# Kernel optimization log

Measured on AMD Instinct MI355X. Metric: run time of the kernel, lower is better.

Reference implementation:

```python
import jax, jax.numpy as jnp
import numpy as np

N_ENT = 200000  # entities per graph (sr and tg)
E = 4_000_000   # triples per graph
R_SR, R_TG, D = 1000, 1200, 128


def _cosine_sim_nbyn(a, b):
    a = a * jax.lax.rsqrt(jnp.sum(a * a, -1, keepdims=True) + 1e-8)
    b = b * jax.lax.rsqrt(jnp.sum(b * b, -1, keepdims=True) + 1e-8)
    return a @ b.T


def _relation_weighting(a, b):
    # pad to square, cosine similarity, max-pool rows/cols (MuGNN RelationWeighting)
    ra, rb = a.shape[0], b.shape[0]
    n = max(ra, rb)
    a_p = jnp.pad(a, ((0, n - ra), (0, 0)))
    b_p = jnp.pad(b, ((0, n - rb), (0, 0)))
    sim = _cosine_sim_nbyn(a_p, b_p)  # [n, n]
    return jnp.max(sim, axis=1)[:ra], jnp.max(sim, axis=0)[:rb]


def _normalize_adj(rows, cols, vals, n):
    # symmetric normalization D^-1/2 A D^-1/2 on COO values
    deg = jax.ops.segment_sum(vals, rows, num_segments=n)
    d_is = jnp.where(deg > 0, jax.lax.rsqrt(jnp.maximum(deg, 1e-12)), 0.0)
    return vals * d_is[rows] * d_is[cols]


def _adjacency_side(head, tail, conf, imp, pca, n):
    # g_func_template: elementwise product of the three aligned sparse matrices
    vals = conf * imp * pca
    # + unit (identity) matrix, then normalize; coords = [edges ; diagonal]
    diag = jnp.arange(n)
    rows = jnp.concatenate([head, diag])
    cols = jnp.concatenate([tail, diag])
    allv = jnp.concatenate([vals, jnp.ones((n,), vals.dtype)])
    return _normalize_adj(rows, cols, allv, n)  # [E+n] COO values


def setup_inputs() -> dict:
    key = jax.random.key(0)
    ks = jax.random.split(key, 14)
    return {
        "rel_emb_sr": jax.random.normal(ks[0], (R_SR, D), jnp.float32),
        "rel_emb_tg": jax.random.normal(ks[1], (R_TG, D), jnp.float32),
        "conf_sr": jax.random.uniform(ks[2], (E,), jnp.float32),
        "imp_sr": jax.random.uniform(ks[3], (E,), jnp.float32),
        "pca_sr": jax.random.uniform(ks[4], (E,), jnp.float32),
        "conf_tg": jax.random.uniform(ks[5], (E,), jnp.float32),
        "imp_tg": jax.random.uniform(ks[6], (E,), jnp.float32),
        "pca_tg": jax.random.uniform(ks[7], (E,), jnp.float32),
        "head_sr": jax.random.randint(ks[8], (E,), 0, N_ENT),
        "tail_sr": jax.random.randint(ks[9], (E,), 0, N_ENT),
        "relation_sr": jax.random.randint(ks[10], (E,), 0, R_SR),
        "head_tg": jax.random.randint(ks[11], (E,), 0, N_ENT),
        "tail_tg": jax.random.randint(ks[12], (E,), 0, N_ENT),
        "relation_tg": jax.random.randint(ks[13], (E,), 0, R_TG),
    }


def reference(rel_emb_sr, rel_emb_tg, conf_sr, imp_sr, pca_sr,
              conf_tg, imp_tg, pca_tg,
              head_sr, tail_sr, relation_sr, head_tg, tail_tg, relation_tg):
    # relation weighting (computed in the original forward; g_func_template
    # discards the gathered relation attention, so relation_sr/tg do not
    # affect the adjacency values)
    rw_sr, rw_tg = _relation_weighting(rel_emb_sr, rel_emb_tg)
    adj_sr = _adjacency_side(head_sr, tail_sr, conf_sr, imp_sr, pca_sr, N_ENT)
    adj_tg = _adjacency_side(head_tg, tail_tg, conf_tg, imp_tg, pca_tg, N_ENT)
    # adjacency returned as normalized COO values on constant coords
    return adj_sr, adj_tg, rw_sr, rw_tg
```

## Files before the change

### kernel.cpp

```cpp
#include <hip/hip_runtime.h>
#include <stdint.h>

#define N_ENT 200000
#define NEDGE 4000000
#define RSR 1000
#define RTG 1200
#define DIM 128

#define NBUCK 400
#define BUCKSZ 500
#define CAP 11264
#define CHUNK 4096
#define NE4 (NEDGE / 4)
#define NBLK 977
#define PER (NEDGE + N_ENT)
#define PER4 (PER / 4)
#define ATILES 16
#define BTILES 19

__device__ __forceinline__ uint32_t to_bf16(float x) {
    uint32_t u = __float_as_uint(x);
    return (u + 0x7FFFu + ((u >> 16) & 1u)) >> 16;
}


__global__ void prep_kernel(const float* __restrict__ emb_sr, const float* __restrict__ emb_tg,
                            float* __restrict__ an, float* __restrict__ bn,
                            float* __restrict__ dis, unsigned* __restrict__ gcount) {
    int blk = blockIdx.x, t = threadIdx.x;
    if (blk < RSR + RTG) {
        const float* src; float* dst; int row;
        if (blk < RSR) { src = emb_sr; dst = an; row = blk; }
        else           { src = emb_tg; dst = bn; row = blk - RSR; }
        float x = src[row * DIM + t];
        __shared__ float sh[DIM];
        sh[t] = x * x;
        __syncthreads();
        for (int off = 64; off > 0; off >>= 1) {
            if (t < off) sh[t] += sh[t + off];
            __syncthreads();
        }
        dst[row * DIM + t] = x * rsqrtf(sh[0] + 1e-8f);
        if (blk == 0)
            for (int i = t; i < 2 * NBUCK; i += DIM) gcount[i] = 0;
    } else {
        int b = blk - (RSR + RTG);
        for (int i = t; i < 1000; i += DIM) dis[b * 1000 + i] = 1.0f;
    }
}


__global__ __launch_bounds__(256) void passA_kernel(
        const float* __restrict__ conf_sr, const float* __restrict__ imp_sr,
        const float* __restrict__ pca_sr,
        const float* __restrict__ conf_tg, const float* __restrict__ imp_tg,
        const float* __restrict__ pca_tg,
        const int* __restrict__ head_sr, const int* __restrict__ head_tg,
        float* __restrict__ out_sr, float* __restrict__ out_tg,
        unsigned* __restrict__ gcount, unsigned* __restrict__ regions) {
    __shared__ unsigned cnt[NBUCK];
    __shared__ unsigned scan_a[512];
    __shared__ unsigned scan_b[512];
    __shared__ unsigned offs[NBUCK];
    __shared__ unsigned gdst[NBUCK];
    __shared__ unsigned stage[CHUNK];
    __shared__ unsigned short aux[CHUNK];

    const int t = threadIdx.x;
    const int side = (int)blockIdx.x >= NBLK;
    const int blk = side ? blockIdx.x - NBLK : blockIdx.x;
    const float4* conf4 = (const float4*)(side ? conf_tg : conf_sr);
    const float4* imp4  = (const float4*)(side ? imp_tg  : imp_sr);
    const float4* pca4  = (const float4*)(side ? pca_tg  : pca_sr);
    const int4*   head4 = (const int4*)(side ? head_tg : head_sr);
    float4*       o4    = (float4*)(side ? out_tg : out_sr);

    for (int i = t; i < NBUCK; i += 256) cnt[i] = 0;
    __syncthreads();

    int bkt[16];
    unsigned rec[16], rnk[16];
#pragma unroll
    for (int i = 0; i < 4; i++) {
        int q = blk * 1024 + t + i * 256;
        if (q < NE4) {
            float4 cf = conf4[q], im = imp4[q], pc = pca4[q];
            int4 hh = head4[q];
            float4 v = make_float4(cf.x * im.x * pc.x, cf.y * im.y * pc.y,
                                   cf.z * im.z * pc.z, cf.w * im.w * pc.w);
            o4[q] = v;
            const int hs[4] = {hh.x, hh.y, hh.z, hh.w};
            const float vs[4] = {v.x, v.y, v.z, v.w};
#pragma unroll
            for (int j = 0; j < 4; j++) {
                int bb = hs[j] / BUCKSZ;
                bkt[i * 4 + j] = bb;
                rec[i * 4 + j] = ((unsigned)(hs[j] - bb * BUCKSZ) << 16) | to_bf16(vs[j]);
                rnk[i * 4 + j] = atomicAdd(&cnt[bb], 1u);
            }
        } else {
#pragma unroll
            for (int j = 0; j < 4; j++) bkt[i * 4 + j] = -1;
        }
    }
    __syncthreads();

    for (int i = t; i < 512; i += 256) scan_a[i] = (i < NBUCK) ? cnt[i] : 0;
    __syncthreads();
    unsigned* src = scan_a;
    unsigned* dst = scan_b;
    for (int s = 1; s < 512; s <<= 1) {
        for (int i = t; i < 512; i += 256)
            dst[i] = src[i] + (i >= s ? src[i - s] : 0u);
        __syncthreads();
        unsigned* tmp = src; src = dst; dst = tmp;
    }
    for (int i = t; i < NBUCK; i += 256) offs[i] = src[i] - cnt[i];
    __syncthreads();

#pragma unroll
    for (int i = 0; i < 16; i++) {
        if (bkt[i] >= 0) {
            unsigned pos = offs[bkt[i]] + rnk[i];
            stage[pos] = rec[i];
            aux[pos] = (unsigned short)bkt[i];
        }
    }
    for (int i = t; i < NBUCK; i += 256) {
        unsigned gb = atomicAdd(&gcount[side * NBUCK + i], cnt[i]);
        gdst[i] = (unsigned)(side * NBUCK + i) * CAP + gb - offs[i];
    }
    __syncthreads();

    unsigned total = src[NBUCK - 1];
    for (int i = t; i < (int)total; i += 256) {
        unsigned b = aux[i];
        unsigned d = gdst[b] + i;
        if (d < (unsigned)(side * NBUCK + b + 1) * CAP) regions[d] = stage[i];
    }
}


__global__ __launch_bounds__(256) void passB_kernel(const unsigned* __restrict__ regions,
                                                    const unsigned* __restrict__ gcount,
                                                    float* __restrict__ dis) {
    __shared__ float bins[BUCKSZ];
    int t = threadIdx.x;
    for (int i = t; i < BUCKSZ; i += 256) bins[i] = 1.0f;
    __syncthreads();
    unsigned n = gcount[blockIdx.x];
    if (n > CAP) n = CAP;
    const unsigned* rp = regions + (size_t)blockIdx.x * CAP;
    for (unsigned i = t; i < n; i += 256) {
        unsigned rec = rp[i];
        atomicAdd(&bins[rec >> 16], __uint_as_float((rec & 0xFFFFu) << 16));
    }
    __syncthreads();
    float* dout = dis + (size_t)blockIdx.x * BUCKSZ;
    for (int i = t; i < BUCKSZ; i += 256) dout[i] = rsqrtf(bins[i]);
}


__global__ void scatter_atomic_kernel(
        const float* __restrict__ conf_sr, const float* __restrict__ imp_sr,
        const float* __restrict__ pca_sr,
        const float* __restrict__ conf_tg, const float* __restrict__ imp_tg,
        const float* __restrict__ pca_tg,
        const int* __restrict__ head_sr, const int* __restrict__ head_tg,
        float* __restrict__ out_sr, float* __restrict__ out_tg,
        float* __restrict__ deg) {
    int e = blockIdx.x * blockDim.x + threadIdx.x;
    if (e < NEDGE) {
        float v = conf_sr[e] * imp_sr[e] * pca_sr[e];
        out_sr[e] = v;
        unsafeAtomicAdd(&deg[head_sr[e]], v);
    } else if (e < 2 * NEDGE) {
        int i = e - NEDGE;
        float v = conf_tg[i] * imp_tg[i] * pca_tg[i];
        out_tg[i] = v;
        unsafeAtomicAdd(&deg[N_ENT + head_tg[i]], v);
    }
}

__global__ void rsqrt_kernel(float* __restrict__ dis) {
    int i = blockIdx.x * blockDim.x + threadIdx.x;
    if (i < 2 * N_ENT) dis[i] = rsqrtf(dis[i]);
}


__global__ __launch_bounds__(256) void finalize_kernel(
        const int* __restrict__ head_sr, const int* __restrict__ tail_sr,
        const int* __restrict__ head_tg, const int* __restrict__ tail_tg,
        const float* __restrict__ dis, float* __restrict__ out) {
    int idx = blockIdx.x * blockDim.x + threadIdx.x;
    if (idx >= 2 * PER4) return;
    int side = idx >= PER4 ? 1 : 0;
    int q = side ? idx - PER4 : idx;
    const float* dg = dis + (size_t)side * N_ENT;
    float4* o = (float4*)(out + (size_t)side * PER);
    if (q < NE4) {
        const int4* hd = (const int4*)(side ? head_tg : head_sr);
        const int4* tl = (const int4*)(side ? tail_tg : tail_sr);
        int4 hh = hd[q];
        int4 tt = tl[q];
        float4 v = o[q];
        v.x *= dg[hh.x] * dg[tt.x];
        v.y *= dg[hh.y] * dg[tt.y];
        v.z *= dg[hh.z] * dg[tt.z];
        v.w *= dg[hh.w] * dg[tt.w];
        o[q] = v;
    } else {
        float4 d = ((const float4*)dg)[q - NE4];
        o[q] = make_float4(d.x * d.x, d.y * d.y, d.z * d.z, d.w * d.w);
    }
}


__global__ __launch_bounds__(256) void pools_tiles_kernel(
        const float* __restrict__ an, const float* __restrict__ bn,
        float* __restrict__ rowpart, float* __restrict__ colpart) {
    __shared__ float sA[64][132];
    __shared__ float sB[64][133];
    __shared__ float rr[64][17];
    __shared__ float cc[64][17];
    int t = threadIdx.x;
    int atile = blockIdx.x % ATILES;
    int btile = blockIdx.x / ATILES;
    for (int idx = t; idx < 64 * 32; idx += 256) {
        int row = idx >> 5, k4 = idx & 31;
        int ga = atile * 64 + row;
        float4 va = (ga < RSR) ? ((const float4*)(an + ga * DIM))[k4]
                               : make_float4(0.f, 0.f, 0.f, 0.f);
        *(float4*)&sA[row][k4 * 4] = va;
        int gb = btile * 64 + row;
        float4 vb = (gb < RTG) ? ((const float4*)(bn + gb * DIM))[k4]
                               : make_float4(0.f, 0.f, 0.f, 0.f);
        sB[row][k4 * 4 + 0] = vb.x; sB[row][k4 * 4 + 1] = vb.y;
        sB[row][k4 * 4 + 2] = vb.z; sB[row][k4 * 4 + 3] = vb.w;
    }
    __syncthreads();
    int tx = t & 15, ty = t >> 4;
    float acc[4][4] = {};
    for (int k4 = 0; k4 < 32; k4++) {
        float4 a4[4];
#pragma unroll
        for (int r = 0; r < 4; r++) a4[r] = *(const float4*)&sA[ty * 4 + r][k4 * 4];
#pragma unroll
        for (int kk = 0; kk < 4; kk++) {
            float bv[4];
#pragma unroll
            for (int c = 0; c < 4; c++) bv[c] = sB[tx * 4 + c][k4 * 4 + kk];
            float av[4];
#pragma unroll
            for (int r = 0; r < 4; r++)
                av[r] = kk == 0 ? a4[r].x : kk == 1 ? a4[r].y : kk == 2 ? a4[r].z : a4[r].w;
#pragma unroll
            for (int r = 0; r < 4; r++)
#pragma unroll
                for (int c = 0; c < 4; c++) acc[r][c] = fmaf(av[r], bv[c], acc[r][c]);
        }
    }
    float rm[4] = {-1e30f, -1e30f, -1e30f, -1e30f};
    float cm[4] = {-1e30f, -1e30f, -1e30f, -1e30f};
#pragma unroll
    for (int r = 0; r < 4; r++)
#pragma unroll
        for (int c = 0; c < 4; c++) {
            bool jok = (btile * 64 + tx * 4 + c) < RTG;
            rm[r] = fmaxf(rm[r], jok ? acc[r][c] : -1e30f);
            cm[c] = fmaxf(cm[c], acc[r][c]);
        }
#pragma unroll
    for (int r = 0; r < 4; r++) rr[ty * 4 + r][tx] = rm[r];
#pragma unroll
    for (int c = 0; c < 4; c++) cc[tx * 4 + c][ty] = cm[c];
    __syncthreads();
    if (t < 64) {
        float m = rr[t][0];
        for (int x = 1; x < 16; x++) m = fmaxf(m, rr[t][x]);
        rowpart[btile * 1024 + atile * 64 + t] = m;
        float m2 = cc[t][0];
        for (int x = 1; x < 16; x++) m2 = fmaxf(m2, cc[t][x]);
        colpart[atile * 1216 + btile * 64 + t] = m2;
    }
}


__global__ void rw_reduce_kernel(const float* __restrict__ rowpart,
                                 const float* __restrict__ colpart,
                                 float* __restrict__ rw_sr, float* __restrict__ rw_tg) {
    int idx = blockIdx.x * blockDim.x + threadIdx.x;
    if (idx < 1024) {
        if (idx < RSR) {
            float m = -1e30f;
            for (int b = 0; b < BTILES; b++) m = fmaxf(m, rowpart[b * 1024 + idx]);
            rw_sr[idx] = m;
        }
    } else {
        int j = idx - 1024;
        if (j < RTG) {
            float m = -1e30f;
            for (int a = 0; a < ATILES; a++) m = fmaxf(m, colpart[a * 1216 + j]);
            rw_tg[j] = fmaxf(m, 0.0f);
        }
    }
}


extern "C" void kernel_launch(void* const* d_in, const int* in_sizes, int n_in,
                              void* d_out, int out_size, void* d_ws, size_t ws_size,
                              hipStream_t stream) {
    const float* rel_emb_sr = (const float*)d_in[0];
    const float* rel_emb_tg = (const float*)d_in[1];
    const float* conf_sr = (const float*)d_in[2];
    const float* imp_sr  = (const float*)d_in[3];
    const float* pca_sr  = (const float*)d_in[4];
    const float* conf_tg = (const float*)d_in[5];
    const float* imp_tg  = (const float*)d_in[6];
    const float* pca_tg  = (const float*)d_in[7];
    const int* head_sr = (const int*)d_in[8];
    const int* tail_sr = (const int*)d_in[9];
    const int* head_tg = (const int*)d_in[11];
    const int* tail_tg = (const int*)d_in[12];

    float* out = (float*)d_out;
    float* out_sr = out;
    float* out_tg = out + PER;
    float* rw_sr  = out + 2 * (size_t)PER;
    float* rw_tg  = rw_sr + RSR;

    float* ws = (float*)d_ws;
    float* an  = ws;
    float* bn  = an + RSR * DIM;
    float* dis = bn + RTG * DIM;
    unsigned* gcount  = (unsigned*)(dis + 2 * N_ENT);
    unsigned* regions = gcount + 2 * NBUCK;
    float* rowpart = (float*)(regions + (size_t)2 * NBUCK * CAP);
    float* colpart = rowpart + BTILES * 1024;

    size_t need = ((size_t)(RSR * DIM + RTG * DIM + 2 * N_ENT + 2 * NBUCK) +
                   (size_t)2 * NBUCK * CAP + BTILES * 1024 + ATILES * 1216) * 4;
    bool bucketed = ws_size >= need;

    hipLaunchKernelGGL(prep_kernel, dim3(RSR + RTG + 400), dim3(DIM), 0, stream,
                       rel_emb_sr, rel_emb_tg, an, bn, dis, gcount);

    if (bucketed) {
        hipLaunchKernelGGL(passA_kernel, dim3(2 * NBLK), dim3(256), 0, stream,
                           conf_sr, imp_sr, pca_sr, conf_tg, imp_tg, pca_tg,
                           head_sr, head_tg, out_sr, out_tg, gcount, regions);
        hipLaunchKernelGGL(passB_kernel, dim3(2 * NBUCK), dim3(256), 0, stream,
                           regions, gcount, dis);
    } else {
        hipLaunchKernelGGL(scatter_atomic_kernel, dim3((2 * NEDGE + 255) / 256), dim3(256),
                           0, stream,
                           conf_sr, imp_sr, pca_sr, conf_tg, imp_tg, pca_tg,
                           head_sr, head_tg, out_sr, out_tg, dis);
        hipLaunchKernelGGL(rsqrt_kernel, dim3((2 * N_ENT + 255) / 256), dim3(256), 0, stream,
                           dis);
    }

    hipLaunchKernelGGL(pools_tiles_kernel, dim3(ATILES * BTILES), dim3(256), 0, stream,
                       an, bn, rowpart, colpart);
    hipLaunchKernelGGL(rw_reduce_kernel, dim3((1024 + 1216 + 255) / 256), dim3(256), 0, stream,
                       rowpart, colpart, rw_sr, rw_tg);

    hipLaunchKernelGGL(finalize_kernel, dim3((2 * PER4 + 255) / 256), dim3(256), 0, stream,
                       head_sr, tail_sr, head_tg, tail_tg, dis, out);
}
```

Baseline: 382.0 us.

## Replace bucketed two-pass degree histogram with direct global float atomics

Removes the shared-memory bucketing pass (bf16-packed records staged into global regions) and the per-bucket reduction pass. Degrees are now accumulated with direct unsafe float atomics into global memory, using float4-vectorized edge loads, followed by a vectorized rsqrt pass. This drops the intermediate region traffic, the block-level scans and one kernel launch, and restores full fp32 precision for the degree sums. In exchange it takes on heavy random global atomic contention across 8M edges.

```diff
diff --git a/kernel.cpp b/kernel.cpp
--- a/kernel.cpp
+++ b/kernel.cpp
@@ -7,26 +7,16 @@
 #define RTG 1200
 #define DIM 128
 
-#define NBUCK 400
-#define BUCKSZ 500
-#define CAP 11264
-#define CHUNK 4096
 #define NE4 (NEDGE / 4)
-#define NBLK 977
 #define PER (NEDGE + N_ENT)
 #define PER4 (PER / 4)
 #define ATILES 16
 #define BTILES 19
 
-__device__ __forceinline__ uint32_t to_bf16(float x) {
-    uint32_t u = __float_as_uint(x);
-    return (u + 0x7FFFu + ((u >> 16) & 1u)) >> 16;
-}
-
 
 __global__ void prep_kernel(const float* __restrict__ emb_sr, const float* __restrict__ emb_tg,
                             float* __restrict__ an, float* __restrict__ bn,
-                            float* __restrict__ dis, unsigned* __restrict__ gcount) {
+                            float* __restrict__ dis) {
     int blk = blockIdx.x, t = threadIdx.x;
     if (blk < RSR + RTG) {
         const float* src; float* dst; int row;
@@ -41,8 +31,6 @@
             __syncthreads();
         }
         dst[row * DIM + t] = x * rsqrtf(sh[0] + 1e-8f);
-        if (blk == 0)
-            for (int i = t; i < 2 * NBUCK; i += DIM) gcount[i] = 0;
     } else {
         int b = blk - (RSR + RTG);
         for (int i = t; i < 1000; i += DIM) dis[b * 1000 + i] = 1.0f;
@@ -50,141 +38,43 @@
 }
 
 
-__global__ __launch_bounds__(256) void passA_kernel(
+__global__ __launch_bounds__(256) void scatter_kernel(
         const float* __restrict__ conf_sr, const float* __restrict__ imp_sr,
         const float* __restrict__ pca_sr,
         const float* __restrict__ conf_tg, const float* __restrict__ imp_tg,
         const float* __restrict__ pca_tg,
         const int* __restrict__ head_sr, const int* __restrict__ head_tg,
         float* __restrict__ out_sr, float* __restrict__ out_tg,
-        unsigned* __restrict__ gcount, unsigned* __restrict__ regions) {
-    __shared__ unsigned cnt[NBUCK];
-    __shared__ unsigned scan_a[512];
-    __shared__ unsigned scan_b[512];
-    __shared__ unsigned offs[NBUCK];
-    __shared__ unsigned gdst[NBUCK];
-    __shared__ unsigned stage[CHUNK];
-    __shared__ unsigned short aux[CHUNK];
-
-    const int t = threadIdx.x;
-    const int side = (int)blockIdx.x >= NBLK;
-    const int blk = side ? blockIdx.x - NBLK : blockIdx.x;
+        float* __restrict__ dis) {
+    int idx = blockIdx.x * 256 + threadIdx.x;
+    if (idx >= 2 * NE4) return;
+    int side = idx >= NE4;
+    int q = side ? idx - NE4 : idx;
     const float4* conf4 = (const float4*)(side ? conf_tg : conf_sr);
     const float4* imp4  = (const float4*)(side ? imp_tg  : imp_sr);
     const float4* pca4  = (const float4*)(side ? pca_tg  : pca_sr);
     const int4*   head4 = (const int4*)(side ? head_tg : head_sr);
     float4*       o4    = (float4*)(side ? out_tg : out_sr);
 
-    for (int i = t; i < NBUCK; i += 256) cnt[i] = 0;
-    __syncthreads();
-
-    int bkt[16];
-    unsigned rec[16], rnk[16];
-#pragma unroll
-    for (int i = 0; i < 4; i++) {
-        int q = blk * 1024 + t + i * 256;
-        if (q < NE4) {
-            float4 cf = conf4[q], im = imp4[q], pc = pca4[q];
-            int4 hh = head4[q];
-            float4 v = make_float4(cf.x * im.x * pc.x, cf.y * im.y * pc.y,
-                                   cf.z * im.z * pc.z, cf.w * im.w * pc.w);
-            o4[q] = v;
-            const int hs[4] = {hh.x, hh.y, hh.z, hh.w};
-            const float vs[4] = {v.x, v.y, v.z, v.w};
-#pragma unroll
-            for (int j = 0; j < 4; j++) {
-                int bb = hs[j] / BUCKSZ;
-                bkt[i * 4 + j] = bb;
-                rec[i * 4 + j] = ((unsigned)(hs[j] - bb * BUCKSZ) << 16) | to_bf16(vs[j]);
-                rnk[i * 4 + j] = atomicAdd(&cnt[bb], 1u);
-            }
-        } else {
-#pragma unroll
-            for (int j = 0; j < 4; j++) bkt[i * 4 + j] = -1;
-        }
-    }
-    __syncthreads();
-
-    for (int i = t; i < 512; i += 256) scan_a[i] = (i < NBUCK) ? cnt[i] : 0;
-    __syncthreads();
-    unsigned* src = scan_a;
-    unsigned* dst = scan_b;
-    for (int s = 1; s < 512; s <<= 1) {
-        for (int i = t; i < 512; i += 256)
-            dst[i] = src[i] + (i >= s ? src[i - s] : 0u);
-        __syncthreads();
-        unsigned* tmp = src; src = dst; dst = tmp;
-    }
-    for (int i = t; i < NBUCK; i += 256) offs[i] = src[i] - cnt[i];
-    __syncthreads();
-
-#pragma unroll
-    for (int i = 0; i < 16; i++) {
-        if (bkt[i] >= 0) {
-            unsigned pos = offs[bkt[i]] + rnk[i];
-            stage[pos] = rec[i];
-            aux[pos] = (unsigned short)bkt[i];
-        }
-    }
-    for (int i = t; i < NBUCK; i += 256) {
-        unsigned gb = atomicAdd(&gcount[side * NBUCK + i], cnt[i]);
-        gdst[i] = (unsigned)(side * NBUCK + i) * CAP + gb - offs[i];
-    }
-    __syncthreads();
-
-    unsigned total = src[NBUCK - 1];
-    for (int i = t; i < (int)total; i += 256) {
-        unsigned b = aux[i];
-        unsigned d = gdst[b] + i;
-        if (d < (unsigned)(side * NBUCK + b + 1) * CAP) regions[d] = stage[i];
-    }
-}
-
-
-__global__ __launch_bounds__(256) void passB_kernel(const unsigned* __restrict__ regions,
-                                                    const unsigned* __restrict__ gcount,
-                                                    float* __restrict__ dis) {
-    __shared__ float bins[BUCKSZ];
-    int t = threadIdx.x;
-    for (int i = t; i < BUCKSZ; i += 256) bins[i] = 1.0f;
-    __syncthreads();
-    unsigned n = gcount[blockIdx.x];
-    if (n > CAP) n = CAP;
-    const unsigned* rp = regions + (size_t)blockIdx.x * CAP;
-    for (unsigned i = t; i < n; i += 256) {
-        unsigned rec = rp[i];
-        atomicAdd(&bins[rec >> 16], __uint_as_float((rec & 0xFFFFu) << 16));
-    }
-    __syncthreads();
-    float* dout = dis + (size_t)blockIdx.x * BUCKSZ;
-    for (int i = t; i < BUCKSZ; i += 256) dout[i] = rsqrtf(bins[i]);
-}
-
-
-__global__ void scatter_atomic_kernel(
-        const float* __restrict__ conf_sr, const float* __restrict__ imp_sr,
-        const float* __restrict__ pca_sr,
-        const float* __restrict__ conf_tg, const float* __restrict__ imp_tg,
-        const float* __restrict__ pca_tg,
-        const int* __restrict__ head_sr, const int* __restrict__ head_tg,
-        float* __restrict__ out_sr, float* __restrict__ out_tg,
-        float* __restrict__ deg) {
-    int e = blockIdx.x * blockDim.x + threadIdx.x;
-    if (e < NEDGE) {
-        float v = conf_sr[e] * imp_sr[e] * pca_sr[e];
-        out_sr[e] = v;
-        unsafeAtomicAdd(&deg[head_sr[e]], v);
-    } else if (e < 2 * NEDGE) {
-        int i = e - NEDGE;
-        float v = conf_tg[i] * imp_tg[i] * pca_tg[i];
-        out_tg[i] = v;
-        unsafeAtomicAdd(&deg[N_ENT + head_tg[i]], v);
-    }
-}
-
-__global__ void rsqrt_kernel(float* __restrict__ dis) {
-    int i = blockIdx.x * blockDim.x + threadIdx.x;
-    if (i < 2 * N_ENT) dis[i] = rsqrtf(dis[i]);
+    float4 cf = conf4[q], im = imp4[q], pc = pca4[q];
+    int4 hh = head4[q];
+    float4 v = make_float4(cf.x * im.x * pc.x, cf.y * im.y * pc.y,
+                           cf.z * im.z * pc.z, cf.w * im.w * pc.w);
+    o4[q] = v;
+    float* dg = dis + (size_t)side * N_ENT;
+    unsafeAtomicAdd(&dg[hh.x], v.x);
+    unsafeAtomicAdd(&dg[hh.y], v.y);
+    unsafeAtomicAdd(&dg[hh.z], v.z);
+    unsafeAtomicAdd(&dg[hh.w], v.w);
+}
+
+
+__global__ __launch_bounds__(256) void rsqrt_kernel(float* __restrict__ dis) {
+    int i = blockIdx.x * 256 + threadIdx.x;
+    if (i < (2 * N_ENT) / 4) {
+        float4 d = ((const float4*)dis)[i];
+        ((float4*)dis)[i] = make_float4(rsqrtf(d.x), rsqrtf(d.y), rsqrtf(d.z), rsqrtf(d.w));
+    }
 }
 
 
@@ -333,32 +223,18 @@
     float* an  = ws;
     float* bn  = an + RSR * DIM;
     float* dis = bn + RTG * DIM;
-    unsigned* gcount  = (unsigned*)(dis + 2 * N_ENT);
-    unsigned* regions = gcount + 2 * NBUCK;
-    float* rowpart = (float*)(regions + (size_t)2 * NBUCK * CAP);
+    float* rowpart = dis + 2 * N_ENT;
     float* colpart = rowpart + BTILES * 1024;
 
-    size_t need = ((size_t)(RSR * DIM + RTG * DIM + 2 * N_ENT + 2 * NBUCK) +
-                   (size_t)2 * NBUCK * CAP + BTILES * 1024 + ATILES * 1216) * 4;
-    bool bucketed = ws_size >= need;
-
     hipLaunchKernelGGL(prep_kernel, dim3(RSR + RTG + 400), dim3(DIM), 0, stream,
-                       rel_emb_sr, rel_emb_tg, an, bn, dis, gcount);
-
-    if (bucketed) {
-        hipLaunchKernelGGL(passA_kernel, dim3(2 * NBLK), dim3(256), 0, stream,
-                           conf_sr, imp_sr, pca_sr, conf_tg, imp_tg, pca_tg,
-                           head_sr, head_tg, out_sr, out_tg, gcount, regions);
-        hipLaunchKernelGGL(passB_kernel, dim3(2 * NBUCK), dim3(256), 0, stream,
-                           regions, gcount, dis);
-    } else {
-        hipLaunchKernelGGL(scatter_atomic_kernel, dim3((2 * NEDGE + 255) / 256), dim3(256),
-                           0, stream,
-                           conf_sr, imp_sr, pca_sr, conf_tg, imp_tg, pca_tg,
-                           head_sr, head_tg, out_sr, out_tg, dis);
-        hipLaunchKernelGGL(rsqrt_kernel, dim3((2 * N_ENT + 255) / 256), dim3(256), 0, stream,
-                           dis);
-    }
+                       rel_emb_sr, rel_emb_tg, an, bn, dis);
+
+    hipLaunchKernelGGL(scatter_kernel, dim3((2 * NE4 + 255) / 256), dim3(256), 0, stream,
+                       conf_sr, imp_sr, pca_sr, conf_tg, imp_tg, pca_tg,
+                       head_sr, head_tg, out_sr, out_tg, dis);
+
+    hipLaunchKernelGGL(rsqrt_kernel, dim3((2 * N_ENT / 4 + 255) / 256), dim3(256), 0, stream,
+                       dis);
 
     hipLaunchKernelGGL(pools_tiles_kernel, dim3(ATILES * BTILES), dim3(256), 0, stream,
                        an, bn, rowpart, colpart);
```

Result: slower. 649.1 us (+69.9%).

## Use power-of-two buckets, 14-bit fixed-point degrees, and wave-shuffle scan in bucketing

Applied to the files above, without the earlier changes.

Switches the degree bucketing to 1024-entity power-of-two buckets, so the bucket is a shift and the bucket id can be recovered from the packed record. That removes the separate aux array. Values are packed as 14-bit fixed point instead of bf16, and the 512-wide Hillis-Steele scan is replaced by a wavefront shuffle scan. The dis initialisation moves out of prep_kernel into passB, which now covers every entity, or into a separate kernel on the fallback path. The fixed-point quantisation changes degree precision, which is a numerical-tolerance risk.

```diff
diff --git a/kernel.cpp b/kernel.cpp
--- a/kernel.cpp
+++ b/kernel.cpp
@@ -7,9 +7,9 @@
 #define RTG 1200
 #define DIM 128
 
-#define NBUCK 400
-#define BUCKSZ 500
-#define CAP 11264
+#define NBUCK 196
+#define BUCKSZ 1024
+#define CAP 22272
 #define CHUNK 4096
 #define NE4 (NEDGE / 4)
 #define NBLK 977
@@ -18,35 +18,25 @@
 #define ATILES 16
 #define BTILES 19
 
-__device__ __forceinline__ uint32_t to_bf16(float x) {
-    uint32_t u = __float_as_uint(x);
-    return (u + 0x7FFFu + ((u >> 16) & 1u)) >> 16;
-}
-
 
 __global__ void prep_kernel(const float* __restrict__ emb_sr, const float* __restrict__ emb_tg,
                             float* __restrict__ an, float* __restrict__ bn,
-                            float* __restrict__ dis, unsigned* __restrict__ gcount) {
+                            unsigned* __restrict__ gcount) {
     int blk = blockIdx.x, t = threadIdx.x;
-    if (blk < RSR + RTG) {
-        const float* src; float* dst; int row;
-        if (blk < RSR) { src = emb_sr; dst = an; row = blk; }
-        else           { src = emb_tg; dst = bn; row = blk - RSR; }
-        float x = src[row * DIM + t];
-        __shared__ float sh[DIM];
-        sh[t] = x * x;
+    const float* src; float* dst; int row;
+    if (blk < RSR) { src = emb_sr; dst = an; row = blk; }
+    else           { src = emb_tg; dst = bn; row = blk - RSR; }
+    float x = src[row * DIM + t];
+    __shared__ float sh[DIM];
+    sh[t] = x * x;
+    __syncthreads();
+    for (int off = 64; off > 0; off >>= 1) {
+        if (t < off) sh[t] += sh[t + off];
         __syncthreads();
-        for (int off = 64; off > 0; off >>= 1) {
-            if (t < off) sh[t] += sh[t + off];
-            __syncthreads();
-        }
-        dst[row * DIM + t] = x * rsqrtf(sh[0] + 1e-8f);
-        if (blk == 0)
-            for (int i = t; i < 2 * NBUCK; i += DIM) gcount[i] = 0;
-    } else {
-        int b = blk - (RSR + RTG);
-        for (int i = t; i < 1000; i += DIM) dis[b * 1000 + i] = 1.0f;
-    }
+    }
+    dst[row * DIM + t] = x * rsqrtf(sh[0] + 1e-8f);
+    if (blk == 0)
+        for (int i = t; i < 2 * NBUCK; i += DIM) gcount[i] = 0;
 }
 
 
@@ -59,12 +49,11 @@
         float* __restrict__ out_sr, float* __restrict__ out_tg,
         unsigned* __restrict__ gcount, unsigned* __restrict__ regions) {
     __shared__ unsigned cnt[NBUCK];
-    __shared__ unsigned scan_a[512];
-    __shared__ unsigned scan_b[512];
     __shared__ unsigned offs[NBUCK];
     __shared__ unsigned gdst[NBUCK];
+    __shared__ unsigned ssum[256];
+    __shared__ unsigned wtot[4];
     __shared__ unsigned stage[CHUNK];
-    __shared__ unsigned short aux[CHUNK];
 
     const int t = threadIdx.x;
     const int side = (int)blockIdx.x >= NBLK;
@@ -93,9 +82,12 @@
             const float vs[4] = {v.x, v.y, v.z, v.w};
 #pragma unroll
             for (int j = 0; j < 4; j++) {
-                int bb = hs[j] / BUCKSZ;
+                int h = hs[j];
+                int bb = h >> 10;
+                unsigned qv = (unsigned)(vs[j] * 16384.f + 0.5f);
+                if (qv > 16383u) qv = 16383u;
                 bkt[i * 4 + j] = bb;
-                rec[i * 4 + j] = ((unsigned)(hs[j] - bb * BUCKSZ) << 16) | to_bf16(vs[j]);
+                rec[i * 4 + j] = ((unsigned)h << 14) | qv;
                 rnk[i * 4 + j] = atomicAdd(&cnt[bb], 1u);
             }
         } else {
@@ -105,38 +97,42 @@
     }
     __syncthreads();
 
-    for (int i = t; i < 512; i += 256) scan_a[i] = (i < NBUCK) ? cnt[i] : 0;
-    __syncthreads();
-    unsigned* src = scan_a;
-    unsigned* dst = scan_b;
-    for (int s = 1; s < 512; s <<= 1) {
-        for (int i = t; i < 512; i += 256)
-            dst[i] = src[i] + (i >= s ? src[i - s] : 0u);
-        __syncthreads();
-        unsigned* tmp = src; src = dst; dst = tmp;
-    }
-    for (int i = t; i < NBUCK; i += 256) offs[i] = src[i] - cnt[i];
-    __syncthreads();
-
-#pragma unroll
-    for (int i = 0; i < 16; i++) {
-        if (bkt[i] >= 0) {
-            unsigned pos = offs[bkt[i]] + rnk[i];
-            stage[pos] = rec[i];
-            aux[pos] = (unsigned short)bkt[i];
-        }
-    }
-    for (int i = t; i < NBUCK; i += 256) {
-        unsigned gb = atomicAdd(&gcount[side * NBUCK + i], cnt[i]);
-        gdst[i] = (unsigned)(side * NBUCK + i) * CAP + gb - offs[i];
-    }
-    __syncthreads();
-
-    unsigned total = src[NBUCK - 1];
+    {
+        int lane = t & 63, w = t >> 6;
+        unsigned s = (t < NBUCK) ? cnt[t] : 0u;
+#pragma unroll
+        for (int d = 1; d < 64; d <<= 1) {
+            unsigned u = __shfl_up(s, d);
+            if (lane >= d) s += u;
+        }
+        if (lane == 63) wtot[w] = s;
+        ssum[t] = s;
+    }
+    __syncthreads();
+    unsigned wb0 = wtot[0];
+    unsigned wb1 = wb0 + wtot[1];
+    unsigned wb2 = wb1 + wtot[2];
+    unsigned total = wb2 + wtot[3];
+    if (t < NBUCK) {
+        int w = t >> 6;
+        unsigned add = (w == 0) ? 0u : (w == 1) ? wb0 : (w == 2) ? wb1 : wb2;
+        unsigned ex = ssum[t] + add - cnt[t];
+        offs[t] = ex;
+        unsigned gb = atomicAdd(&gcount[side * NBUCK + t], cnt[t]);
+        gdst[t] = (unsigned)(side * NBUCK + t) * CAP + gb - ex;
+    }
+    __syncthreads();
+
+#pragma unroll
+    for (int i = 0; i < 16; i++)
+        if (bkt[i] >= 0) stage[offs[bkt[i]] + rnk[i]] = rec[i];
+    __syncthreads();
+
     for (int i = t; i < (int)total; i += 256) {
-        unsigned b = aux[i];
+        unsigned r = stage[i];
+        unsigned b = r >> 24;
         unsigned d = gdst[b] + i;
-        if (d < (unsigned)(side * NBUCK + b + 1) * CAP) regions[d] = stage[i];
+        if (d < (unsigned)(side * NBUCK + b + 1) * CAP) regions[d] = r;
     }
 }
 
@@ -146,20 +142,33 @@
                                                     float* __restrict__ dis) {
     __shared__ float bins[BUCKSZ];
     int t = threadIdx.x;
-    for (int i = t; i < BUCKSZ; i += 256) bins[i] = 1.0f;
-    __syncthreads();
-    unsigned n = gcount[blockIdx.x];
+    int sb = blockIdx.x;
+    for (int i = t; i < BUCKSZ; i += 256) bins[i] = 0.f;
+    __syncthreads();
+    unsigned n = gcount[sb];
     if (n > CAP) n = CAP;
-    const unsigned* rp = regions + (size_t)blockIdx.x * CAP;
+    const unsigned* rp = regions + (size_t)sb * CAP;
     for (unsigned i = t; i < n; i += 256) {
-        unsigned rec = rp[i];
-        atomicAdd(&bins[rec >> 16], __uint_as_float((rec & 0xFFFFu) << 16));
-    }
-    __syncthreads();
-    float* dout = dis + (size_t)blockIdx.x * BUCKSZ;
-    for (int i = t; i < BUCKSZ; i += 256) dout[i] = rsqrtf(bins[i]);
-}
-
+        unsigned r = rp[i];
+        atomicAdd(&bins[(r >> 14) & (BUCKSZ - 1)], (float)(r & 16383u) * (1.f / 16384.f));
+    }
+    __syncthreads();
+    int side = sb >= NBUCK;
+    int b = side ? sb - NBUCK : sb;
+    int base = b * BUCKSZ;
+    float* dout = dis + (size_t)side * N_ENT;
+    for (int i = t; i < BUCKSZ; i += 256) {
+        int e = base + i;
+        if (e < N_ENT) dout[e] = rsqrtf(1.0f + bins[i]);
+    }
+}
+
+
+__global__ void deg_init_kernel(float* __restrict__ dis) {
+    int i = blockIdx.x * 256 + threadIdx.x;
+    if (i < (2 * N_ENT) / 4)
+        ((float4*)dis)[i] = make_float4(1.f, 1.f, 1.f, 1.f);
+}
 
 __global__ void scatter_atomic_kernel(
         const float* __restrict__ conf_sr, const float* __restrict__ imp_sr,
@@ -334,16 +343,16 @@
     float* bn  = an + RSR * DIM;
     float* dis = bn + RTG * DIM;
     unsigned* gcount  = (unsigned*)(dis + 2 * N_ENT);
-    unsigned* regions = gcount + 2 * NBUCK;
+    unsigned* regions = gcount + 512;
     float* rowpart = (float*)(regions + (size_t)2 * NBUCK * CAP);
     float* colpart = rowpart + BTILES * 1024;
 
-    size_t need = ((size_t)(RSR * DIM + RTG * DIM + 2 * N_ENT + 2 * NBUCK) +
+    size_t need = ((size_t)(RSR * DIM + RTG * DIM + 2 * N_ENT + 512) +
                    (size_t)2 * NBUCK * CAP + BTILES * 1024 + ATILES * 1216) * 4;
     bool bucketed = ws_size >= need;
 
-    hipLaunchKernelGGL(prep_kernel, dim3(RSR + RTG + 400), dim3(DIM), 0, stream,
-                       rel_emb_sr, rel_emb_tg, an, bn, dis, gcount);
+    hipLaunchKernelGGL(prep_kernel, dim3(RSR + RTG), dim3(DIM), 0, stream,
+                       rel_emb_sr, rel_emb_tg, an, bn, gcount);
 
     if (bucketed) {
         hipLaunchKernelGGL(passA_kernel, dim3(2 * NBLK), dim3(256), 0, stream,
@@ -352,6 +361,8 @@
         hipLaunchKernelGGL(passB_kernel, dim3(2 * NBUCK), dim3(256), 0, stream,
                            regions, gcount, dis);
     } else {
+        hipLaunchKernelGGL(deg_init_kernel, dim3((2 * N_ENT / 4 + 255) / 256), dim3(256),
+                           0, stream, dis);
         hipLaunchKernelGGL(scatter_atomic_kernel, dim3((2 * NEDGE + 255) / 256), dim3(256),
                            0, stream,
                            conf_sr, imp_sr, pca_sr, conf_tg, imp_tg, pca_tg,
```

Measured after the change: 374.6 us. About the same (-1.9%).
